# Performance work log

Hardware: AMD Instinct MI355X
Metric: run time of the kernel (lower is better)

Reference implementation:

```python
import jax, jax.numpy as jnp
import numpy as np

B, T, D = 16, 512, 256
HH = D // 2   # per-direction hidden of bidirectional GRU
G, Z, R, NA = 32, 8, 16, 18


def _gru_step(h, x, wih, whh, bih, bhh):
    # torch.nn.GRUCell math
    gi = x @ wih.T + bih
    gh = h @ whh.T + bhh
    ir, iz, inn = jnp.split(gi, 3, axis=-1)
    hr, hz, hn = jnp.split(gh, 3, axis=-1)
    r = jax.nn.sigmoid(ir + hr)
    z = jax.nn.sigmoid(iz + hz)
    n = jnp.tanh(inn + r * hn)
    return (1.0 - z) * n + z * h


def _gru_seq(x_tbd, wih, whh, bih, bhh):
    h0 = jnp.zeros((x_tbd.shape[1], whh.shape[1]), x_tbd.dtype)
    def step(h, x):
        h = _gru_step(h, x, wih, whh, bih, bhh)
        return h, h
    _, hs = jax.lax.scan(step, h0, x_tbd)
    return hs  # (T, B, H)


def setup_inputs() -> dict:
    key = jax.random.key(0)
    ks = jax.random.split(key, 26)
    rn = lambda k, s, sc: jax.random.normal(k, s, jnp.float32) * sc
    d = {
        'e_seq': rn(ks[0], (B, T, D), 1.0),
        'eps':   rn(ks[1], (B, T, Z), 1.0),
        # acausal bidirectional GRU (fwd + bwd cells)
        'wih_f': rn(ks[2], (3 * HH, D), D ** -0.5),  'whh_f': rn(ks[3], (3 * HH, HH), HH ** -0.5),
        'bih_f': jnp.zeros((3 * HH,)), 'bhh_f': jnp.zeros((3 * HH,)),
        'wih_b': rn(ks[4], (3 * HH, D), D ** -0.5),  'whh_b': rn(ks[5], (3 * HH, HH), HH ** -0.5),
        'bih_b': jnp.zeros((3 * HH,)), 'bhh_b': jnp.zeros((3 * HH,)),
        # controller encoder GRUCell(2D -> G) + heads
        'wih_e': rn(ks[6], (3 * G, 2 * D), (2 * D) ** -0.5), 'whh_e': rn(ks[7], (3 * G, G), G ** -0.5),
        'bih_e': jnp.zeros((3 * G,)), 'bhh_e': jnp.zeros((3 * G,)),
        'mu_w': rn(ks[8], (Z, G), G ** -0.5),  'mu_b': jnp.zeros((Z,)),
        'lv_w': rn(ks[9], (Z, G), G ** -0.5),  'lv_b': jnp.zeros((Z,)),
        # switching unit MLP (D+G+Z -> 64 -> 1)
        'sw1_w': rn(ks[10], (64, D + G + Z), (D + G + Z) ** -0.5), 'sw1_b': jnp.zeros((64,)),
        'sw2_w': rn(ks[11], (1, 64), 64 ** -0.5), 'sw2_b': jnp.zeros((1,)),
        # decoder hypernet (Z -> 32 -> 2*D*R)
        'dec1_w': rn(ks[12], (32, Z), Z ** -0.5), 'dec1_b': jnp.zeros((32,)),
        'dec2_w': rn(ks[13], (2 * D * R, 32), 32 ** -0.5), 'dec2_b': jnp.zeros((2 * D * R,)),
        # final norm + action head
        'ln_g': jnp.ones((D,)), 'ln_b': jnp.zeros((D,)),
        'head_w': rn(ks[14], (NA, D), D ** -0.5), 'head_b': jnp.zeros((NA,)),
    }
    return d


def _forward(e_seq, eps, wih_f, whh_f, bih_f, bhh_f, wih_b, whh_b, bih_b, bhh_b,
             wih_e, whh_e, bih_e, bhh_e, mu_w, mu_b, lv_w, lv_b,
             sw1_w, sw1_b, sw2_w, sw2_b, dec1_w, dec1_b, dec2_w, dec2_b,
             ln_g, ln_b, head_w, head_b):
    Bz, Tt, Dm = e_seq.shape
    e_tbd = jnp.swapaxes(e_seq, 0, 1)                      # (T, B, D)
    # AcausalEmbedder: bidirectional GRU
    fwd = _gru_seq(e_tbd, wih_f, whh_f, bih_f, bhh_f)
    bwd = _gru_seq(e_tbd[::-1], wih_b, whh_b, bih_b, bhh_b)[::-1]
    s_tbd = jnp.concatenate([fwd, bwd], axis=-1)           # (T, B, D)
    eps_tbd = jnp.swapaxes(eps, 0, 1)

    h0 = jnp.zeros((Bz, whh_e.shape[1]), e_seq.dtype)
    z0 = jnp.zeros((Bz, mu_w.shape[0]), e_seq.dtype)

    def step(carry, xs):
        h, z_prev = carry
        e_t, s_t, eps_t = xs
        h = _gru_step(h, jnp.concatenate([e_t, s_t], axis=-1), wih_e, whh_e, bih_e, bhh_e)
        mu = h @ mu_w.T + mu_b
        logvar = h @ lv_w.T + lv_b
        # switching unit uses updated h (causal)
        hid = jnp.tanh(jnp.concatenate([e_t, h, z_prev], axis=-1) @ sw1_w.T + sw1_b)
        beta = jax.nn.sigmoid(hid @ sw2_w.T + sw2_b)       # (B, 1)
        z = beta * (mu + jnp.exp(0.5 * logvar) * eps_t) + (1.0 - beta) * z_prev
        return (h, jax.lax.stop_gradient(z)), (mu, logvar, beta, z)

    _, (mu_t, lv_t, be_t, z_t) = jax.lax.scan(step, (h0, z0), (e_tbd, s_tbd, eps_tbd))
    mu_seq = jnp.swapaxes(mu_t, 0, 1)
    logvar_seq = jnp.swapaxes(lv_t, 0, 1)
    beta_seq = jnp.swapaxes(be_t, 0, 1)
    z_seq = jnp.swapaxes(z_t, 0, 1)                        # (B, T, Z)

    # ControllerDecoder: z -> (A, Bm); apply U = A @ Bm^T without materializing U
    hmid = jnp.tanh(z_seq @ dec1_w.T + dec1_b)
    ab = hmid @ dec2_w.T + dec2_b                          # (B, T, 2*D*R)
    DR = ab.shape[-1] // 2
    A = ab[..., :DR].reshape(Bz, Tt, Dm, -1)               # (B, T, D, R)
    Bm = ab[..., DR:].reshape(Bz, Tt, Dm, -1)
    tmp = jnp.einsum('btdr,btd->btr', Bm, e_seq)
    perturbed = e_seq + jnp.einsum('btdr,btr->btd', A, tmp)

    # final LayerNorm + action head on obs positions
    mean = perturbed.mean(-1, keepdims=True)
    var = perturbed.var(-1, keepdims=True)
    xn = (perturbed - mean) * jax.lax.rsqrt(var + 1e-5) * ln_g + ln_b
    logits = xn @ head_w.T + head_b                        # (B, T, NA)
    return logits, mu_seq, logvar_seq, beta_seq, z_seq


def reference(e_seq, eps, wih_f, whh_f, bih_f, bhh_f, wih_b, whh_b, bih_b, bhh_b,
              wih_e, whh_e, bih_e, bhh_e, mu_w, mu_b, lv_w, lv_b,
              sw1_w, sw1_b, sw2_w, sw2_b, dec1_w, dec1_b, dec2_w, dec2_b,
              ln_g, ln_b, head_w, head_b):
    return _forward(e_seq, eps, wih_f, whh_f, bih_f, bhh_f, wih_b, whh_b, bih_b, bhh_b,
                    wih_e, whh_e, bih_e, bhh_e, mu_w, mu_b, lv_w, lv_b,
                    sw1_w, sw1_b, sw2_w, sw2_b, dec1_w, dec1_b, dec2_w, dec2_b,
                    ln_g, ln_b, head_w, head_b)
```

## Files before the change

### kernel.cpp

```cpp
#include <hip/hip_runtime.h>

#define TT 512
#define BB 16
#define DD 256
#define HHH 128
#define GG 32
#define ZZ 8
#define RR_ 16
#define NAA 18

typedef _Float16 h2v __attribute__((ext_vector_type(2)));
typedef __attribute__((ext_vector_type(4))) float f4;
typedef __attribute__((ext_vector_type(4))) int i4;

__device__ __forceinline__ float sigmoid_(float x) { return 1.f / (1.f + __expf(-x)); }
__device__ __forceinline__ float tanh_(float x) { float e = __expf(2.f * x); return 1.f - 2.f / (e + 1.f); }
__device__ __forceinline__ float dot4(float4 a, float4 b) {
    return a.x * b.x + a.y * b.y + a.z * b.z + a.w * b.w;
}
__device__ __forceinline__ h2v u2h2(unsigned u) { union { unsigned u; h2v h; } c; c.u = u; return c.h; }

__device__ __forceinline__ void lds_barrier() {
    asm volatile("s_waitcnt lgkmcnt(0)" ::: "memory");
    __builtin_amdgcn_s_barrier();
}

template <int CTRL, int RM, int BM, bool BC>
__device__ __forceinline__ float dpp_add_f(float v) {
    return v + __int_as_float(__builtin_amdgcn_update_dpp(0, __float_as_int(v), CTRL, RM, BM, BC));
}
__device__ __forceinline__ float wave_sum_bcast(float p) {
    p = dpp_add_f<0x111, 0xf, 0xf, true>(p);
    p = dpp_add_f<0x112, 0xf, 0xf, true>(p);
    p = dpp_add_f<0x114, 0xf, 0xf, true>(p);
    p = dpp_add_f<0x118, 0xf, 0xf, true>(p);
    p = dpp_add_f<0x142, 0xa, 0xf, false>(p);
    p = dpp_add_f<0x143, 0xc, 0xf, false>(p);
    return __int_as_float(__builtin_amdgcn_readlane(__float_as_int(p), 63));
}
__device__ __forceinline__ float quad_sum(float v) {
    v = dpp_add_f<0xB1, 0xf, 0xf, true>(v);
    v = dpp_add_f<0x4E, 0xf, 0xf, true>(v);
    return v;
}
__device__ __forceinline__ float rdlane(float v, int l) {
    return __int_as_float(__builtin_amdgcn_readlane(__float_as_int(v), l));
}

__global__ __launch_bounds__(256) void pack_w(
    const float* __restrict__ wf, const float* __restrict__ wb,
    const float* __restrict__ we,
    unsigned* __restrict__ pk, unsigned* __restrict__ pk_e)
{
    int i = blockIdx.x * 256 + threadIdx.x;
    if (i < 49152) {
        int dir = i / 24576; int r = i % 24576;
        int w = r / 3072;    int r2 = r % 3072;
        int T = r2 / 1024;   int r3 = r2 % 1024;
        int kt = r3 / 256;   int r4 = r3 % 256;
        int lane = r4 / 4;   int jd = r4 % 4;
        const float* wsrc = dir ? wb : wf;
        int row = T * 128 + 16 * w + (lane & 15);
        int k0 = kt * 32 + (lane >> 4) * 8 + 2 * jd;
        union { _Float16 h[2]; unsigned u; } c;
        c.h[0] = (_Float16)wsrc[row * 128 + k0];
        c.h[1] = (_Float16)wsrc[row * 128 + k0 + 1];
        pk[i] = c.u;
    } else if (i < 50688) {
        int ie = i - 49152;
        int s = ie / 384;  int rem = ie % 384;
        int k = rem / 12;  int e = rem % 12;
        int j = e / 4;     int m = e % 4;
        int row = j * 32 + k, k0 = 8 * s + 2 * m;
        union { _Float16 h[2]; unsigned u; } c;
        c.h[0] = (_Float16)we[row * 32 + k0];
        c.h[1] = (_Float16)we[row * 32 + k0 + 1];
        pk_e[ie] = c.u;
    }
}

__global__ __launch_bounds__(256) void gemm_k(
    const float* __restrict__ A, int K, const float* __restrict__ W, int ldw,
    const float* __restrict__ bias, float* __restrict__ Out, int ldout, int N, int accFlag)
{
    __shared__ float At[64][36];
    __shared__ float Wt[32][36];
    int row0 = blockIdx.x * 64, n0 = blockIdx.y * 32;
    int tid = threadIdx.x;
    int tx = tid & 15, ty = tid >> 4;
    float acc[4][2] = {};
    for (int k0 = 0; k0 < K; k0 += 32) {
        #pragma unroll
        for (int i = 0; i < 8; ++i) {
            int idx = tid + i * 256; int rr = idx >> 5, kk = idx & 31;
            At[rr][kk] = A[(size_t)(row0 + rr) * K + k0 + kk];
        }
        #pragma unroll
        for (int i = 0; i < 4; ++i) {
            int idx = tid + i * 256; int nn = idx >> 5, kk = idx & 31;
            Wt[nn][kk] = (n0 + nn < N) ? W[(size_t)(n0 + nn) * ldw + k0 + kk] : 0.f;
        }
        __syncthreads();
        #pragma unroll
        for (int kk = 0; kk < 32; kk += 4) {
            float4 w0 = *(const float4*)&Wt[tx][kk];
            float4 w1 = *(const float4*)&Wt[tx + 16][kk];
            #pragma unroll
            for (int rr = 0; rr < 4; ++rr) {
                float4 av = *(const float4*)&At[ty * 4 + rr][kk];
                acc[rr][0] += dot4(av, w0);
                acc[rr][1] += dot4(av, w1);
            }
        }
        __syncthreads();
    }
    #pragma unroll
    for (int cc = 0; cc < 2; ++cc) {
        int n = n0 + tx + cc * 16;
        if (n < N) {
            float badd = bias ? bias[n] : 0.f;
            #pragma unroll
            for (int rr = 0; rr < 4; ++rr) {
                int row = row0 + ty * 4 + rr;
                float v = acc[rr][cc] + badd;
                if (accFlag) Out[(size_t)row * ldout + n] += v;
                else         Out[(size_t)row * ldout + n] = v;
            }
        }
    }
}

__global__ __launch_bounds__(256) void gemm_gi(
    const float* __restrict__ A,
    const float* __restrict__ wf, const float* __restrict__ bf, float* __restrict__ of,
    const float* __restrict__ wb, const float* __restrict__ bb, float* __restrict__ ob)
{
    __shared__ float At[64][36];
    __shared__ float Wt[32][36];
    int y = blockIdx.y;
    const float* W; const float* bias; float* Out; int n0;
    if (y < 12) { W = wf; bias = bf; Out = of; n0 = y * 32; }
    else        { W = wb; bias = bb; Out = ob; n0 = (y - 12) * 32; }
    int row0 = blockIdx.x * 64;
    int tid = threadIdx.x;
    int tx = tid & 15, ty = tid >> 4;
    float acc[4][2] = {};
    for (int k0 = 0; k0 < 256; k0 += 32) {
        #pragma unroll
        for (int i = 0; i < 8; ++i) {
            int idx = tid + i * 256; int rr = idx >> 5, kk = idx & 31;
            At[rr][kk] = A[(size_t)(row0 + rr) * 256 + k0 + kk];
        }
        #pragma unroll
        for (int i = 0; i < 4; ++i) {
            int idx = tid + i * 256; int nn = idx >> 5, kk = idx & 31;
            Wt[nn][kk] = W[(size_t)(n0 + nn) * 256 + k0 + kk];
        }
        __syncthreads();
        #pragma unroll
        for (int kk = 0; kk < 32; kk += 4) {
            float4 w0 = *(const float4*)&Wt[tx][kk];
            float4 w1 = *(const float4*)&Wt[tx + 16][kk];
            #pragma unroll
            for (int rr = 0; rr < 4; ++rr) {
                float4 av = *(const float4*)&At[ty * 4 + rr][kk];
                acc[rr][0] += dot4(av, w0);
                acc[rr][1] += dot4(av, w1);
            }
        }
        __syncthreads();
    }
    #pragma unroll
    for (int cc = 0; cc < 2; ++cc) {
        int n = n0 + tx + cc * 16;
        float badd = bias[n];
        #pragma unroll
        for (int rr = 0; rr < 4; ++rr) {
            int row = row0 + ty * 4 + rr;
            Out[(size_t)row * 384 + n] = acc[rr][cc] + badd;
        }
    }
}

struct __align__(16) SmGru { _Float16 hb[2][128]; };
struct __align__(16) SmGemm { float At[64][36]; float Wt[32][36]; };
union __align__(16) SmU { SmGru g; SmGemm m; };

__device__ __forceinline__ void gemm_tile512(
    const float* __restrict__ A, int K, const float* __restrict__ W, int ldw,
    const float* __restrict__ bias, float* __restrict__ Out, int ldout, int N,
    int row0, int n0, SmGemm& sm)
{
    int tid = threadIdx.x;
    int tx = tid & 31, ty = tid >> 5;
    float acc[4] = {};
    for (int k0 = 0; k0 < K; k0 += 32) {
        #pragma unroll
        for (int i = 0; i < 4; ++i) {
            int idx = tid + i * 512; int rr = idx >> 5, kk = idx & 31;
            sm.At[rr][kk] = A[(size_t)(row0 + rr) * K + k0 + kk];
        }
        #pragma unroll
        for (int i = 0; i < 2; ++i) {
            int idx = tid + i * 512; int nn = idx >> 5, kk = idx & 31;
            sm.Wt[nn][kk] = (n0 + nn < N) ? W[(size_t)(n0 + nn) * ldw + k0 + kk] : 0.f;
        }
        __syncthreads();
        #pragma unroll
        for (int kk = 0; kk < 32; kk += 4) {
            float4 w0 = *(const float4*)&sm.Wt[tx][kk];
            #pragma unroll
            for (int rr = 0; rr < 4; ++rr) {
                float4 av = *(const float4*)&sm.At[ty * 4 + rr][kk];
                acc[rr] += dot4(av, w0);
            }
        }
        __syncthreads();
    }
    int n = n0 + tx;
    if (n < N) {
        float badd = bias ? bias[n] : 0.f;
        #pragma unroll
        for (int rr = 0; rr < 4; ++rr)
            Out[(size_t)(row0 + ty * 4 + rr) * ldout + n] = acc[rr] + badd;
    }
}

__global__ __launch_bounds__(512, 2) void gru_fused(
    const float* __restrict__ gi_f, const float* __restrict__ gi_b,
    const unsigned* __restrict__ pk,
    const float* __restrict__ bhh_f, const float* __restrict__ bhh_b,
    float* __restrict__ s_seq,
    const float* __restrict__ e,
    const float* __restrict__ wih_e, const float* __restrict__ bih_e, float* __restrict__ gie,
    const float* __restrict__ sw1_w, const float* __restrict__ sw1_b, float* __restrict__ swe)
{
    __shared__ SmU sm;
    int bx = blockIdx.x;
    if (bx >= 416) {
        int t = bx - 416;
        gemm_tile512(e, 256, sw1_w, 296, sw1_b, swe, 64, 64, (t & 127) * 64, (t >> 7) * 32, sm.m);
        return;
    }
    if (bx >= 32) {
        int t = bx - 32;
        gemm_tile512(e, 256, wih_e, 512, bih_e, gie, 96, 96, (t & 127) * 64, (t >> 7) * 32, sm.m);
        return;
    }

    int dir = bx >> 4, b = bx & 15;
    const float* gi  = dir ? gi_b  : gi_f;
    const float* bhh = dir ? bhh_b : bhh_f;
    int tid = threadIdx.x;
    int w = tid >> 6;
    int lane = tid & 63;
    int quad = lane >> 4;
    int c = lane & 15;
    int j = 16 * w + c;

    i4 bf[3][4];
    #pragma unroll
    for (int T = 0; T < 3; ++T)
        #pragma unroll
        for (int kt = 0; kt < 4; ++kt)
            bf[T][kt] = *(const i4*)(pk + (size_t)((((dir * 8 + w) * 3 + T) * 4 + kt) * 64 + lane) * 4);
    #pragma unroll
    for (int T = 0; T < 3; ++T)
        #pragma unroll
        for (int kt = 0; kt < 4; ++kt)
            asm volatile("" : "+a"(bf[T][kt]));

    if (tid < 128) sm.g.hb[0][tid] = (_Float16)0.f;

    float bhr = 0.f, bhz = 0.f, bhn = 0.f;
    float gra = 0.f, gza = 0.f, gna = 0.f;
    float grb = 0.f, gzb = 0.f, gnb = 0.f;
    float hreg = 0.f;
    if (lane < 16) {
        bhr = bhh[j]; bhz = bhh[128 + j]; bhn = bhh[256 + j];
        int t0 = dir ? 511 : 0;
        int t1 = dir ? 510 : 1;
        size_t p0 = (size_t)(b * TT + t0) * 384;
        size_t p1 = (size_t)(b * TT + t1) * 384;
        gra = gi[p0 + j]; gza = gi[p0 + 128 + j]; gna = gi[p0 + 256 + j];
        grb = gi[p1 + j]; gzb = gi[p1 + 128 + j]; gnb = gi[p1 + 256 + j];
    }
    __syncthreads();

    int cur = 0;
    auto body = [&](int step, float& gr, float& gz, float& gn) {
        i4 af[4];
        #pragma unroll
        for (int kt = 0; kt < 4; ++kt)
            af[kt] = *(const i4*)(&sm.g.hb[cur][kt * 32 + quad * 8]);
        f4 accr = {0.f, 0.f, 0.f, 0.f};
        f4 accz = {0.f, 0.f, 0.f, 0.f};
        f4 accn = {0.f, 0.f, 0.f, 0.f};
        asm volatile("s_nop 3" : "+v"(accr), "+v"(accz), "+v"(accn));
        #pragma unroll
        for (int kt = 0; kt < 4; ++kt) {
            asm volatile("v_mfma_f32_16x16x32_f16 %0, %1, %2, %0" : "+v"(accr) : "v"(af[kt]), "a"(bf[0][kt]));
            asm volatile("v_mfma_f32_16x16x32_f16 %0, %1, %2, %0" : "+v"(accz) : "v"(af[kt]), "a"(bf[1][kt]));
            asm volatile("v_mfma_f32_16x16x32_f16 %0, %1, %2, %0" : "+v"(accn) : "v"(af[kt]), "a"(bf[2][kt]));
        }
        asm volatile("s_nop 7\n\ts_nop 7" : "+v"(accr), "+v"(accz), "+v"(accn));
        if (lane < 16) {
            int t = dir ? (511 - step) : step;
            int p = b * TT + t;
            float r = sigmoid_(gr + bhr + accr[0]);
            float z = sigmoid_(gz + bhz + accz[0]);
            float n = tanh_(gn + r * (bhn + accn[0]));
            float hn = (1.f - z) * n + z * hreg;
            hreg = hn;
            sm.g.hb[cur ^ 1][j] = (_Float16)hn;
            s_seq[(size_t)p * 256 + dir * 128 + j] = hn;
            int s2 = step + 2;
            int tp = (s2 < 512) ? (dir ? (511 - s2) : s2) : t;
            size_t p2 = (size_t)(b * TT + tp) * 384;
            gr = gi[p2 + j]; gz = gi[p2 + 128 + j]; gn = gi[p2 + 256 + j];
        }
        lds_barrier();
        cur ^= 1;
    };

    for (int step = 0; step < 512; step += 2) {
        body(step,     gra, gza, gna);
        body(step + 1, grb, gzb, gnb);
    }
}

__global__ __launch_bounds__(128, 1) void ctrl_fused(
    const float* __restrict__ gie, const unsigned* __restrict__ pk_e,
    const float* __restrict__ bhh_e,
    const float* __restrict__ mu_w, const float* __restrict__ mu_b,
    const float* __restrict__ lv_w, const float* __restrict__ lv_b,
    const float* __restrict__ sw1_w, const float* __restrict__ sw2_w,
    const float* __restrict__ sw2_b,
    const float* __restrict__ swe,
    const float* __restrict__ eps,
    float* __restrict__ out_mu, float* __restrict__ out_lv,
    float* __restrict__ beta_o, float* __restrict__ z_o)
{
    int b = blockIdx.x;
    int tid = threadIdx.x;
    int wid = tid >> 6;
    int lane = tid & 63;
    int pbase = b * TT;

    __shared__ __align__(16) _Float16 hb[16][32];
    __shared__ __align__(16) float    hf[16][32];

    int k = lane >> 1, s2 = lane & 1;
    unsigned wg[24];
    float bhr = 0.f, bhz = 0.f, bhn = 0.f, hreg = 0.f;
    float g1[8] = {}, g2[8] = {}, g3[8] = {};
    if (wid == 0) {
        #pragma unroll
        for (int ss = 0; ss < 2; ++ss) {
            const uint4* wp = (const uint4*)(pk_e + ((size_t)((2 * s2 + ss) * 32) + k) * 12);
            #pragma unroll
            for (int i = 0; i < 3; ++i) {
                uint4 u = wp[i];
                wg[12 * ss + 4 * i + 0] = u.x;
                wg[12 * ss + 4 * i + 1] = u.y;
                wg[12 * ss + 4 * i + 2] = u.z;
                wg[12 * ss + 4 * i + 3] = u.w;
            }
        }
        if (lane < 32) hb[15][lane] = (_Float16)0.f;
        if (s2 == 0) {
            bhr = bhh_e[k]; bhz = bhh_e[32 + k]; bhn = bhh_e[64 + k];
            #pragma unroll
            for (int i = 0; i < 8; ++i) {
                size_t p = (size_t)(pbase + i) * 96;
                g1[i] = gie[p + k]; g2[i] = gie[p + 32 + k]; g3[i] = gie[p + 64 + k];
            }
        }
    }

    int x = lane >> 3, kind = (lane >> 2) & 1, s = lane & 3;
    float4 swh4[8];
    float4 wz0v = {0,0,0,0}, wz1v = {0,0,0,0}, mlw0 = {0,0,0,0}, mlw1 = {0,0,0,0};
    float w2 = 0.f, sb2 = 0.f, mlb = 0.f;
    float4 zr0 = {0.f, 0.f, 0.f, 0.f}, zr1 = {0.f, 0.f, 0.f, 0.f};
    float hp[8] = {}, ep[8] = {};
    if (wid == 1) {
        #pragma unroll
        for (int i = 0; i < 8; ++i)
            swh4[i] = *(const float4*)(sw1_w + (size_t)lane * 296 + 256 + 4 * i);
        wz0v = *(const float4*)(sw1_w + (size_t)lane * 296 + 288);
        wz1v = *(const float4*)(sw1_w + (size_t)lane * 296 + 292);
        w2 = sw2_w[lane];
        sb2 = sw2_b[0];
        const float* mw = kind ? lv_w : mu_w;
        mlw0 = *(const float4*)(mw + x * 32 + 8 * s);
        mlw1 = *(const float4*)(mw + x * 32 + 8 * s + 4);
        mlb = kind ? lv_b[x] : mu_b[x];
        #pragma unroll
        for (int i = 0; i < 8; ++i) {
            hp[i] = swe[(size_t)(pbase + i) * 64 + lane];
            ep[i] = eps[(size_t)(pbase + i) * 8 + x];
        }
    }
    __syncthreads();

    auto prod_step = [&](int t, float& ga, float& gb, float& gc) {
        const uint4* hv = (const uint4*)(&hb[(t - 1) & 15][16 * s2]);
        uint4 hA = hv[0], hB = hv[1];
        unsigned hw[8] = {hA.x, hA.y, hA.z, hA.w, hB.x, hB.y, hB.z, hB.w};
        float a0 = 0.f, a1 = 0.f, a2 = 0.f, c0 = 0.f, c1 = 0.f, c2 = 0.f;
        #pragma unroll
        for (int m = 0; m < 4; ++m) {
            a0 = __builtin_amdgcn_fdot2(u2h2(wg[m]),      u2h2(hw[m]),     a0, false);
            a1 = __builtin_amdgcn_fdot2(u2h2(wg[4 + m]),  u2h2(hw[m]),     a1, false);
            a2 = __builtin_amdgcn_fdot2(u2h2(wg[8 + m]),  u2h2(hw[m]),     a2, false);
            c0 = __builtin_amdgcn_fdot2(u2h2(wg[12 + m]), u2h2(hw[4 + m]), c0, false);
            c1 = __builtin_amdgcn_fdot2(u2h2(wg[16 + m]), u2h2(hw[4 + m]), c1, false);
            c2 = __builtin_amdgcn_fdot2(u2h2(wg[20 + m]), u2h2(hw[4 + m]), c2, false);
        }
        a0 += c0; a1 += c1; a2 += c2;
        a0 = dpp_add_f<0xB1, 0xf, 0xf, true>(a0);
        a1 = dpp_add_f<0xB1, 0xf, 0xf, true>(a1);
        a2 = dpp_add_f<0xB1, 0xf, 0xf, true>(a2);
        if (s2 == 0) {
            float r = sigmoid_(ga + bhr + a0);
            float z = sigmoid_(gb + bhz + a1);
            float n = tanh_(gc + r * (bhn + a2));
            float hn = (1.f - z) * n + z * hreg;
            hreg = hn;
            hb[t & 15][k] = (_Float16)hn;
            hf[t & 15][k] = hn;
            int t8 = (t + 8 < 512) ? (t + 8) : t;
            size_t p2 = (size_t)(pbase + t8) * 96;
            ga = gie[p2 + k]; gb = gie[p2 + 32 + k]; gc = gie[p2 + 64 + k];
        }
    };

    auto cons_step = [&](int t, float& hpi, float& epi) {
        int sl = t & 15;
        const float4* hv4 = (const float4*)(&hf[sl][0]);
        float4 h0 = hv4[0], h1 = hv4[1], h2 = hv4[2], h3 = hv4[3];
        float4 h4 = hv4[4], h5 = hv4[5], h6 = hv4[6], h7 = hv4[7];
        float d0 = dot4(swh4[0], h0) + dot4(swh4[1], h1);
        float d1 = dot4(swh4[2], h2) + dot4(swh4[3], h3);
        float d2 = dot4(swh4[4], h4) + dot4(swh4[5], h5);
        float d3 = dot4(swh4[6], h6) + dot4(swh4[7], h7);
        float hsum = (d0 + d1) + (d2 + d3);
        float4 hs0 = *(const float4*)(&hf[sl][8 * s]);
        float4 hs1 = *(const float4*)(&hf[sl][8 * s + 4]);
        float pacc = quad_sum(dot4(mlw0, hs0) + dot4(mlw1, hs1));
        float v = pacc + mlb;
        float other = __int_as_float(__builtin_amdgcn_ds_swizzle(__float_as_int(v), 0x101F));
        float muv = kind ? other : v;
        float lvv = kind ? v : other;
        float cand = muv + __expf(0.5f * lvv) * epi;
        float sc0 = rdlane(cand, 0),  sc1 = rdlane(cand, 8);
        float sc2 = rdlane(cand, 16), sc3 = rdlane(cand, 24);
        float sc4 = rdlane(cand, 32), sc5 = rdlane(cand, 40);
        float sc6 = rdlane(cand, 48), sc7 = rdlane(cand, 56);
        float az = dot4(wz0v, zr0) + dot4(wz1v, zr1);
        float a = (hpi + hsum) + az;
        float hid = tanh_(a);
        float beta = sigmoid_(wave_sum_bcast(w2 * hid) + sb2);
        float omb = 1.f - beta;
        zr0.x = beta * sc0 + omb * zr0.x; zr0.y = beta * sc1 + omb * zr0.y;
        zr0.z = beta * sc2 + omb * zr0.z; zr0.w = beta * sc3 + omb * zr0.w;
        zr1.x = beta * sc4 + omb * zr1.x; zr1.y = beta * sc5 + omb * zr1.y;
        zr1.z = beta * sc6 + omb * zr1.z; zr1.w = beta * sc7 + omb * zr1.w;
        int p = pbase + t;
        if (lane == 0) {
            beta_o[p] = beta;
            *(float4*)(z_o + (size_t)p * 8)     = zr0;
            *(float4*)(z_o + (size_t)p * 8 + 4) = zr1;
        }
        if ((lane & 7) == 0) out_mu[(size_t)p * 8 + x] = muv;
        if ((lane & 7) == 4) out_lv[(size_t)p * 8 + x] = lvv;
        int t8 = (t + 8 < 512) ? (t + 8) : t;
        hpi = swe[(size_t)(pbase + t8) * 64 + lane];
        epi = eps[(size_t)(pbase + t8) * 8 + x];
    };

    for (int ph = 0; ph < 65; ++ph) {
        if (wid == 0) {
            if (ph < 64) {
                int t0 = ph * 8;
                #pragma unroll
                for (int i = 0; i < 8; ++i)
                    prod_step(t0 + i, g1[i], g2[i], g3[i]);
            }
        } else {
            if (ph >= 1) {
                int t0 = (ph - 1) * 8;
                #pragma unroll
                for (int i = 0; i < 8; ++i)
                    cons_step(t0 + i, hp[i], ep[i]);
            }
        }
        lds_barrier();
    }
}

__global__ __launch_bounds__(256, 3) void decoder_final(
    const float* __restrict__ e_seq, const float* __restrict__ z_o,
    const float* __restrict__ dec1_w, const float* __restrict__ dec1_b,
    const float* __restrict__ dec2_w, const float* __restrict__ dec2_b,
    const float* __restrict__ ln_g, const float* __restrict__ ln_b,
    const float* __restrict__ head_w, const float* __restrict__ head_b,
    float* __restrict__ logits)
{
    __shared__ __align__(16) float e_l[8][256];
    __shared__ __align__(16) float hmid[8][32];
    __shared__ float zl[8][8];
    __shared__ float tmpw[8][16];
    __shared__ __align__(16) float partb[2048];
    __shared__ float red1[8][16];
    __shared__ float red2[8][16];
    __shared__ float stats[8][2];
    int tid = threadIdx.x;
    int p0 = blockIdx.x * 8;

    {
        const float4* eg = (const float4*)(e_seq + (size_t)p0 * 256);
        float4* el4 = (float4*)&e_l[0][0];
        el4[tid] = eg[tid];
        el4[tid + 256] = eg[tid + 256];
        if (tid < 64) ((float*)zl)[tid] = z_o[p0 * 8 + tid];
    }
    __syncthreads();
    {
        int pp = tid >> 5, g = tid & 31;
        float a = dec1_b[g];
        #pragma unroll
        for (int x = 0; x < 8; ++x) a += dec1_w[g * 8 + x] * zl[pp][x];
        hmid[pp][g] = tanh_(a);
    }
    __syncthreads();
    {
        int r = tid & 15, dgrp = tid >> 4;
        float acc[8];
        #pragma unroll
        for (int pp = 0; pp < 8; ++pp) acc[pp] = 0.f;
        for (int iblk = 0; iblk < 8; ++iblk) {
            float4 wr[2][8]; float wb[2]; int dd[2];
            #pragma unroll
            for (int ii = 0; ii < 2; ++ii) {
                int d = dgrp + 16 * (iblk * 2 + ii);
                dd[ii] = d;
                int row = 4096 + d * 16 + r;
                const float4* wp = (const float4*)(dec2_w + (size_t)row * 32);
                #pragma unroll
                for (int g = 0; g < 8; ++g) wr[ii][g] = wp[g];
                wb[ii] = dec2_b[row];
            }
            #pragma unroll 1
            for (int pp = 0; pp < 8; ++pp) {
                const float4* hv = (const float4*)hmid[pp];
                float b0 = wb[0], b1 = wb[1];
                #pragma unroll
                for (int g = 0; g < 8; ++g) {
                    float4 hh = hv[g];
                    b0 += dot4(wr[0][g], hh);
                    b1 += dot4(wr[1][g], hh);
                }
                acc[pp] += b0 * e_l[pp][dd[0]] + b1 * e_l[pp][dd[1]];
            }
        }
        #pragma unroll
        for (int pp = 0; pp < 8; ++pp) partb[(pp * 16 + r) * 16 + dgrp] = acc[pp];
    }
    __syncthreads();
    if (tid < 128) {
        int pp = tid >> 4, rr = tid & 15;
        float s = 0.f;
        #pragma unroll
        for (int dg = 0; dg < 16; ++dg) s += partb[(pp * 16 + rr) * 16 + dg];
        tmpw[pp][rr] = s;
    }
    __syncthreads();
    {
        int d = tid;
        float po[8];
        #pragma unroll
        for (int pp = 0; pp < 8; ++pp) po[pp] = e_l[pp][d];
        for (int rblk = 0; rblk < 8; ++rblk) {
            float4 wr[2][8]; float wb[2];
            #pragma unroll
            for (int ii = 0; ii < 2; ++ii) {
                int row = d * 16 + rblk * 2 + ii;
                const float4* wp = (const float4*)(dec2_w + (size_t)row * 32);
                #pragma unroll
                for (int g = 0; g < 8; ++g) wr[ii][g] = wp[g];
                wb[ii] = dec2_b[row];
            }
            #pragma unroll 1
            for (int pp = 0; pp < 8; ++pp) {
                const float4* hv = (const float4*)hmid[pp];
                float a0 = wb[0], a1 = wb[1];
                #pragma unroll
                for (int g = 0; g < 8; ++g) {
                    float4 hh = hv[g];
                    a0 += dot4(wr[0][g], hh);
                    a1 += dot4(wr[1][g], hh);
                }
                po[pp] += a0 * tmpw[pp][rblk * 2] + a1 * tmpw[pp][rblk * 2 + 1];
            }
        }
        #pragma unroll
        for (int pp = 0; pp < 8; ++pp) partb[pp * 256 + d] = po[pp];
    }
    __syncthreads();
    if (tid < 128) {
        int pp = tid >> 4, c = tid & 15;
        float s = 0.f, s2 = 0.f;
        #pragma unroll
        for (int i = 0; i < 16; ++i) { float v = partb[pp * 256 + c * 16 + i]; s += v; s2 += v * v; }
        red1[pp][c] = s; red2[pp][c] = s2;
    }
    __syncthreads();
    if (tid < 8) {
        float s = 0.f, s2 = 0.f;
        #pragma unroll
        for (int c = 0; c < 16; ++c) { s += red1[tid][c]; s2 += red2[tid][c]; }
        float mean = s * (1.f / 256.f);
        float var = s2 * (1.f / 256.f) - mean * mean;
        stats[tid][0] = mean;
        stats[tid][1] = rsqrtf(var + 1e-5f);
    }
    __syncthreads();
    {
        int d = tid;
        float g = ln_g[d], bln = ln_b[d];
        #pragma unroll
        for (int pp = 0; pp < 8; ++pp) {
            float v = (partb[pp * 256 + d] - stats[pp][0]) * stats[pp][1];
            partb[pp * 256 + d] = v * g + bln;
        }
    }
    __syncthreads();
    if (tid < 144) {
        int pp = tid / 18, na = tid - pp * 18;
        float a = head_b[na];
        for (int d2 = 0; d2 < 256; ++d2)
            a += partb[pp * 256 + d2] * head_w[na * 256 + d2];
        logits[(size_t)(p0 + pp) * 18 + na] = a;
    }
}

extern "C" void kernel_launch(void* const* d_in, const int* in_sizes, int n_in,
                              void* d_out, int out_size, void* d_ws, size_t ws_size,
                              hipStream_t stream) {
    (void)in_sizes; (void)n_in; (void)out_size; (void)ws_size;
    const float* e     = (const float*)d_in[0];
    const float* eps   = (const float*)d_in[1];
    const float* wih_f = (const float*)d_in[2];
    const float* whh_f = (const float*)d_in[3];
    const float* bih_f = (const float*)d_in[4];
    const float* bhh_f = (const float*)d_in[5];
    const float* wih_b = (const float*)d_in[6];
    const float* whh_b = (const float*)d_in[7];
    const float* bih_b = (const float*)d_in[8];
    const float* bhh_b = (const float*)d_in[9];
    const float* wih_e = (const float*)d_in[10];
    const float* whh_e = (const float*)d_in[11];
    const float* bih_e = (const float*)d_in[12];
    const float* bhh_e = (const float*)d_in[13];
    const float* mu_w  = (const float*)d_in[14];
    const float* mu_b  = (const float*)d_in[15];
    const float* lv_w  = (const float*)d_in[16];
    const float* lv_b  = (const float*)d_in[17];
    const float* sw1_w = (const float*)d_in[18];
    const float* sw1_b = (const float*)d_in[19];
    const float* sw2_w = (const float*)d_in[20];
    const float* sw2_b = (const float*)d_in[21];
    const float* dec1_w = (const float*)d_in[22];
    const float* dec1_b = (const float*)d_in[23];
    const float* dec2_w = (const float*)d_in[24];
    const float* dec2_b = (const float*)d_in[25];
    const float* ln_g  = (const float*)d_in[26];
    const float* ln_b  = (const float*)d_in[27];
    const float* head_w = (const float*)d_in[28];
    const float* head_b = (const float*)d_in[29];

    float* ws    = (float*)d_ws;
    float* gi_f  = ws;
    float* gi_b  = gi_f + 3145728;
    float* gie   = gi_b + 3145728;
    float* swe   = gie + 786432;
    float* s_seq = swe + 524288;
    float* h_seq = s_seq + 2097152;
    unsigned* pk   = (unsigned*)(h_seq + 262144);
    unsigned* pk_e = pk + 49152;
    (void)h_seq;

    float* out       = (float*)d_out;
    float* out_logit = out;
    float* out_mu    = out + 147456;
    float* out_lv    = out + 212992;
    float* out_beta  = out + 278528;
    float* out_z     = out + 286720;

    pack_w<<<198, 256, 0, stream>>>(whh_f, whh_b, whh_e, pk, pk_e);
    gemm_gi<<<dim3(128, 24), 256, 0, stream>>>(e, wih_f, bih_f, gi_f, wih_b, bih_b, gi_b);
    gru_fused<<<672, 512, 0, stream>>>(gi_f, gi_b, pk, bhh_f, bhh_b, s_seq,
                                       e, wih_e, bih_e, gie, sw1_w, sw1_b, swe);
    gemm_k<<<dim3(128, 3), 256, 0, stream>>>(s_seq, 256, wih_e + 256, 512, nullptr, gie, 96, 96, 1);
    ctrl_fused<<<16, 128, 0, stream>>>(gie, pk_e, bhh_e, mu_w, mu_b, lv_w, lv_b,
                                       sw1_w, sw2_w, sw2_b, swe, eps,
                                       out_mu, out_lv, out_beta, out_z);
    decoder_final<<<1024, 256, 0, stream>>>(e, out_z, dec1_w, dec1_b, dec2_w, dec2_b,
                                            ln_g, ln_b, head_w, head_b, out_logit);
}
```

Baseline: 898.3 us.

## Halve GRU block to 4 waves and double controller phase length

The bidirectional GRU recurrence block drops from 8 to 4 waves. Each wave now holds two 16-column weight tiles in AGPRs and issues twice as many MFMAs per step, so fewer waves take part in each per-step barrier. The side GEMM tiles in that kernel are reshaped for 256 threads, with each thread computing two output columns. The controller producer/consumer pipeline now runs 16 steps per phase instead of 8, using a 32-slot ring buffer and deeper prefetch, which halves the number of block barriers. The cost is a longer serial MFMA chain per wave on the recurrence critical path and more registers per thread.

```diff
diff --git a/kernel.cpp b/kernel.cpp
--- a/kernel.cpp
+++ b/kernel.cpp
@@ -186,47 +186,52 @@
 struct __align__(16) SmGemm { float At[64][36]; float Wt[32][36]; };
 union __align__(16) SmU { SmGru g; SmGemm m; };
 
-__device__ __forceinline__ void gemm_tile512(
+__device__ __forceinline__ void gemm_tile256(
     const float* __restrict__ A, int K, const float* __restrict__ W, int ldw,
     const float* __restrict__ bias, float* __restrict__ Out, int ldout, int N,
     int row0, int n0, SmGemm& sm)
 {
     int tid = threadIdx.x;
-    int tx = tid & 31, ty = tid >> 5;
-    float acc[4] = {};
+    int tx = tid & 15, ty = tid >> 4;
+    float acc[4][2] = {};
     for (int k0 = 0; k0 < K; k0 += 32) {
         #pragma unroll
+        for (int i = 0; i < 8; ++i) {
+            int idx = tid + i * 256; int rr = idx >> 5, kk = idx & 31;
+            sm.At[rr][kk] = A[(size_t)(row0 + rr) * K + k0 + kk];
+        }
+        #pragma unroll
         for (int i = 0; i < 4; ++i) {
-            int idx = tid + i * 512; int rr = idx >> 5, kk = idx & 31;
-            sm.At[rr][kk] = A[(size_t)(row0 + rr) * K + k0 + kk];
-        }
-        #pragma unroll
-        for (int i = 0; i < 2; ++i) {
-            int idx = tid + i * 512; int nn = idx >> 5, kk = idx & 31;
+            int idx = tid + i * 256; int nn = idx >> 5, kk = idx & 31;
             sm.Wt[nn][kk] = (n0 + nn < N) ? W[(size_t)(n0 + nn) * ldw + k0 + kk] : 0.f;
         }
         __syncthreads();
         #pragma unroll
         for (int kk = 0; kk < 32; kk += 4) {
             float4 w0 = *(const float4*)&sm.Wt[tx][kk];
+            float4 w1 = *(const float4*)&sm.Wt[tx + 16][kk];
             #pragma unroll
             for (int rr = 0; rr < 4; ++rr) {
                 float4 av = *(const float4*)&sm.At[ty * 4 + rr][kk];
-                acc[rr] += dot4(av, w0);
+                acc[rr][0] += dot4(av, w0);
+                acc[rr][1] += dot4(av, w1);
             }
         }
         __syncthreads();
     }
-    int n = n0 + tx;
-    if (n < N) {
-        float badd = bias ? bias[n] : 0.f;
-        #pragma unroll
-        for (int rr = 0; rr < 4; ++rr)
-            Out[(size_t)(row0 + ty * 4 + rr) * ldout + n] = acc[rr] + badd;
-    }
-}
-
-__global__ __launch_bounds__(512, 2) void gru_fused(
+    #pragma unroll
+    for (int cc = 0; cc < 2; ++cc) {
+        int n = n0 + tx + cc * 16;
+        if (n < N) {
+            float badd = bias[n];
+            #pragma unroll
+            for (int rr = 0; rr < 4; ++rr)
+                Out[(size_t)(row0 + ty * 4 + rr) * ldout + n] = acc[rr][cc] + badd;
+        }
+    }
+}
+
+__global__ __launch_bounds__(256, 2) void gru_fused(
     const float* __restrict__ gi_f, const float* __restrict__ gi_b,
     const unsigned* __restrict__ pk,
     const float* __restrict__ bhh_f, const float* __restrict__ bhh_b,
@@ -239,12 +244,12 @@
     int bx = blockIdx.x;
     if (bx >= 416) {
         int t = bx - 416;
-        gemm_tile512(e, 256, sw1_w, 296, sw1_b, swe, 64, 64, (t & 127) * 64, (t >> 7) * 32, sm.m);
+        gemm_tile256(e, 256, sw1_w, 296, sw1_b, swe, 64, 64, (t & 127) * 64, (t >> 7) * 32, sm.m);
         return;
     }
     if (bx >= 32) {
         int t = bx - 32;
-        gemm_tile512(e, 256, wih_e, 512, bih_e, gie, 96, 96, (t & 127) * 64, (t >> 7) * 32, sm.m);
+        gemm_tile256(e, 256, wih_e, 512, bih_e, gie, 96, 96, (t & 127) * 64, (t >> 7) * 32, sm.m);
         return;
     }
 
@@ -255,20 +260,23 @@
     int w = tid >> 6;
     int lane = tid & 63;
     int quad = lane >> 4;
-    int c = lane & 15;
-    int j = 16 * w + c;
-
-    i4 bf[3][4];
+    int j = 32 * w + (lane & 31);
+
+    i4 bf[2][3][4];
     #pragma unroll
-    for (int T = 0; T < 3; ++T)
-        #pragma unroll
-        for (int kt = 0; kt < 4; ++kt)
-            bf[T][kt] = *(const i4*)(pk + (size_t)((((dir * 8 + w) * 3 + T) * 4 + kt) * 64 + lane) * 4);
+    for (int tt = 0; tt < 2; ++tt)
+        #pragma unroll
+        for (int T = 0; T < 3; ++T)
+            #pragma unroll
+            for (int kt = 0; kt < 4; ++kt)
+                bf[tt][T][kt] = *(const i4*)(pk + (size_t)((((dir * 8 + 2 * w + tt) * 3 + T) * 4 + kt) * 64 + lane) * 4);
     #pragma unroll
-    for (int T = 0; T < 3; ++T)
-        #pragma unroll
-        for (int kt = 0; kt < 4; ++kt)
-            asm volatile("" : "+a"(bf[T][kt]));
+    for (int tt = 0; tt < 2; ++tt)
+        #pragma unroll
+        for (int T = 0; T < 3; ++T)
+            #pragma unroll
+            for (int kt = 0; kt < 4; ++kt)
+                asm volatile("" : "+a"(bf[tt][T][kt]));
 
     if (tid < 128) sm.g.hb[0][tid] = (_Float16)0.f;
 
@@ -276,7 +284,7 @@
     float gra = 0.f, gza = 0.f, gna = 0.f;
     float grb = 0.f, gzb = 0.f, gnb = 0.f;
     float hreg = 0.f;
-    if (lane < 16) {
+    if (lane < 32) {
         bhr = bhh[j]; bhz = bhh[128 + j]; bhn = bhh[256 + j];
         int t0 = dir ? 511 : 0;
         int t1 = dir ? 510 : 1;
@@ -293,23 +301,32 @@
         #pragma unroll
         for (int kt = 0; kt < 4; ++kt)
             af[kt] = *(const i4*)(&sm.g.hb[cur][kt * 32 + quad * 8]);
-        f4 accr = {0.f, 0.f, 0.f, 0.f};
-        f4 accz = {0.f, 0.f, 0.f, 0.f};
-        f4 accn = {0.f, 0.f, 0.f, 0.f};
-        asm volatile("s_nop 3" : "+v"(accr), "+v"(accz), "+v"(accn));
+        f4 accr0 = {0.f, 0.f, 0.f, 0.f}, accr1 = {0.f, 0.f, 0.f, 0.f};
+        f4 accz0 = {0.f, 0.f, 0.f, 0.f}, accz1 = {0.f, 0.f, 0.f, 0.f};
+        f4 accn0 = {0.f, 0.f, 0.f, 0.f}, accn1 = {0.f, 0.f, 0.f, 0.f};
+        asm volatile("s_nop 3" : "+v"(accr0), "+v"(accz0), "+v"(accn0),
+                                 "+v"(accr1), "+v"(accz1), "+v"(accn1));
         #pragma unroll
         for (int kt = 0; kt < 4; ++kt) {
-            asm volatile("v_mfma_f32_16x16x32_f16 %0, %1, %2, %0" : "+v"(accr) : "v"(af[kt]), "a"(bf[0][kt]));
-            asm volatile("v_mfma_f32_16x16x32_f16 %0, %1, %2, %0" : "+v"(accz) : "v"(af[kt]), "a"(bf[1][kt]));
-            asm volatile("v_mfma_f32_16x16x32_f16 %0, %1, %2, %0" : "+v"(accn) : "v"(af[kt]), "a"(bf[2][kt]));
-        }
-        asm volatile("s_nop 7\n\ts_nop 7" : "+v"(accr), "+v"(accz), "+v"(accn));
-        if (lane < 16) {
+            asm volatile("v_mfma_f32_16x16x32_f16 %0, %1, %2, %0" : "+v"(accr0) : "v"(af[kt]), "a"(bf[0][0][kt]));
+            asm volatile("v_mfma_f32_16x16x32_f16 %0, %1, %2, %0" : "+v"(accz0) : "v"(af[kt]), "a"(bf[0][1][kt]));
+            asm volatile("v_mfma_f32_16x16x32_f16 %0, %1, %2, %0" : "+v"(accn0) : "v"(af[kt]), "a"(bf[0][2][kt]));
+            asm volatile("v_mfma_f32_16x16x32_f16 %0, %1, %2, %0" : "+v"(accr1) : "v"(af[kt]), "a"(bf[1][0][kt]));
+            asm volatile("v_mfma_f32_16x16x32_f16 %0, %1, %2, %0" : "+v"(accz1) : "v"(af[kt]), "a"(bf[1][1][kt]));
+            asm volatile("v_mfma_f32_16x16x32_f16 %0, %1, %2, %0" : "+v"(accn1) : "v"(af[kt]), "a"(bf[1][2][kt]));
+        }
+        asm volatile("s_nop 7\n\ts_nop 7" : "+v"(accr0), "+v"(accz0), "+v"(accn0),
+                                            "+v"(accr1), "+v"(accz1), "+v"(accn1));
+        if (lane < 32) {
             int t = dir ? (511 - step) : step;
             int p = b * TT + t;
-            float r = sigmoid_(gr + bhr + accr[0]);
-            float z = sigmoid_(gz + bhz + accz[0]);
-            float n = tanh_(gn + r * (bhn + accn[0]));
+            bool hi = lane >= 16;
+            float ar = hi ? accr1[0] : accr0[0];
+            float az = hi ? accz1[0] : accz0[0];
+            float an = hi ? accn1[0] : accn0[0];
+            float r = sigmoid_(gr + bhr + ar);
+            float z = sigmoid_(gz + bhz + az);
+            float n = tanh_(gn + r * (bhn + an));
             float hn = (1.f - z) * n + z * hreg;
             hreg = hn;
             sm.g.hb[cur ^ 1][j] = (_Float16)hn;
@@ -347,13 +364,13 @@
     int lane = tid & 63;
     int pbase = b * TT;
 
-    __shared__ __align__(16) _Float16 hb[16][32];
-    __shared__ __align__(16) float    hf[16][32];
+    __shared__ __align__(16) _Float16 hb[32][32];
+    __shared__ __align__(16) float    hf[32][32];
 
     int k = lane >> 1, s2 = lane & 1;
     unsigned wg[24];
     float bhr = 0.f, bhz = 0.f, bhn = 0.f, hreg = 0.f;
-    float g1[8] = {}, g2[8] = {}, g3[8] = {};
+    float g1[16] = {}, g2[16] = {}, g3[16] = {};
     if (wid == 0) {
         #pragma unroll
         for (int ss = 0; ss < 2; ++ss) {
@@ -367,11 +384,11 @@
                 wg[12 * ss + 4 * i + 3] = u.w;
             }
         }
-        if (lane < 32) hb[15][lane] = (_Float16)0.f;
+        if (lane < 32) hb[31][lane] = (_Float16)0.f;
         if (s2 == 0) {
             bhr = bhh_e[k]; bhz = bhh_e[32 + k]; bhn = bhh_e[64 + k];
             #pragma unroll
-            for (int i = 0; i < 8; ++i) {
+            for (int i = 0; i < 16; ++i) {
                 size_t p = (size_t)(pbase + i) * 96;
                 g1[i] = gie[p + k]; g2[i] = gie[p + 32 + k]; g3[i] = gie[p + 64 + k];
             }
@@ -383,7 +400,7 @@
     float4 wz0v = {0,0,0,0}, wz1v = {0,0,0,0}, mlw0 = {0,0,0,0}, mlw1 = {0,0,0,0};
     float w2 = 0.f, sb2 = 0.f, mlb = 0.f;
     float4 zr0 = {0.f, 0.f, 0.f, 0.f}, zr1 = {0.f, 0.f, 0.f, 0.f};
-    float hp[8] = {}, ep[8] = {};
+    float hp[16] = {}, ep[16] = {};
     if (wid == 1) {
         #pragma unroll
         for (int i = 0; i < 8; ++i)
@@ -397,7 +414,7 @@
         mlw1 = *(const float4*)(mw + x * 32 + 8 * s + 4);
         mlb = kind ? lv_b[x] : mu_b[x];
         #pragma unroll
-        for (int i = 0; i < 8; ++i) {
+        for (int i = 0; i < 16; ++i) {
             hp[i] = swe[(size_t)(pbase + i) * 64 + lane];
             ep[i] = eps[(size_t)(pbase + i) * 8 + x];
         }
@@ -405,7 +422,7 @@
     __syncthreads();
 
     auto prod_step = [&](int t, float& ga, float& gb, float& gc) {
-        const uint4* hv = (const uint4*)(&hb[(t - 1) & 15][16 * s2]);
+        const uint4* hv = (const uint4*)(&hb[(t - 1) & 31][16 * s2]);
         uint4 hA = hv[0], hB = hv[1];
         unsigned hw[8] = {hA.x, hA.y, hA.z, hA.w, hB.x, hB.y, hB.z, hB.w};
         float a0 = 0.f, a1 = 0.f, a2 = 0.f, c0 = 0.f, c1 = 0.f, c2 = 0.f;
@@ -428,16 +445,16 @@
             float n = tanh_(gc + r * (bhn + a2));
             float hn = (1.f - z) * n + z * hreg;
             hreg = hn;
-            hb[t & 15][k] = (_Float16)hn;
-            hf[t & 15][k] = hn;
-            int t8 = (t + 8 < 512) ? (t + 8) : t;
-            size_t p2 = (size_t)(pbase + t8) * 96;
+            hb[t & 31][k] = (_Float16)hn;
+            hf[t & 31][k] = hn;
+            int t16 = (t + 16 < 512) ? (t + 16) : t;
+            size_t p2 = (size_t)(pbase + t16) * 96;
             ga = gie[p2 + k]; gb = gie[p2 + 32 + k]; gc = gie[p2 + 64 + k];
         }
     };
 
     auto cons_step = [&](int t, float& hpi, float& epi) {
-        int sl = t & 15;
+        int sl = t & 31;
         const float4* hv4 = (const float4*)(&hf[sl][0]);
         float4 h0 = hv4[0], h1 = hv4[1], h2 = hv4[2], h3 = hv4[3];
         float4 h4 = hv4[4], h5 = hv4[5], h6 = hv4[6], h7 = hv4[7];
@@ -475,24 +492,24 @@
         }
         if ((lane & 7) == 0) out_mu[(size_t)p * 8 + x] = muv;
         if ((lane & 7) == 4) out_lv[(size_t)p * 8 + x] = lvv;
-        int t8 = (t + 8 < 512) ? (t + 8) : t;
-        hpi = swe[(size_t)(pbase + t8) * 64 + lane];
-        epi = eps[(size_t)(pbase + t8) * 8 + x];
+        int t16 = (t + 16 < 512) ? (t + 16) : t;
+        hpi = swe[(size_t)(pbase + t16) * 64 + lane];
+        epi = eps[(size_t)(pbase + t16) * 8 + x];
     };
 
-    for (int ph = 0; ph < 65; ++ph) {
+    for (int ph = 0; ph < 33; ++ph) {
         if (wid == 0) {
-            if (ph < 64) {
-                int t0 = ph * 8;
+            if (ph < 32) {
+                int t0 = ph * 16;
                 #pragma unroll
-                for (int i = 0; i < 8; ++i)
+                for (int i = 0; i < 16; ++i)
                     prod_step(t0 + i, g1[i], g2[i], g3[i]);
             }
         } else {
             if (ph >= 1) {
-                int t0 = (ph - 1) * 8;
+                int t0 = (ph - 1) * 16;
                 #pragma unroll
-                for (int i = 0; i < 8; ++i)
+                for (int i = 0; i < 16; ++i)
                     cons_step(t0 + i, hp[i], ep[i]);
             }
         }
@@ -701,7 +718,7 @@
 
     pack_w<<<198, 256, 0, stream>>>(whh_f, whh_b, whh_e, pk, pk_e);
     gemm_gi<<<dim3(128, 24), 256, 0, stream>>>(e, wih_f, bih_f, gi_f, wih_b, bih_b, gi_b);
-    gru_fused<<<672, 512, 0, stream>>>(gi_f, gi_b, pk, bhh_f, bhh_b, s_seq,
+    gru_fused<<<672, 256, 0, stream>>>(gi_f, gi_b, pk, bhh_f, bhh_b, s_seq,
                                        e, wih_e, bih_e, gie, sw1_w, sw1_b, swe);
     gemm_k<<<dim3(128, 3), 256, 0, stream>>>(s_seq, 256, wih_e + 256, 512, nullptr, gie, 96, 96, 1);
     ctrl_fused<<<16, 128, 0, stream>>>(gie, pk_e, bhh_e, mu_w, mu_b, lv_w, lv_b,
```

Result: no change. 888.6 us (-1.1%).
